# Optimization experiments

Hardware: AMD Instinct MI355X
Metric: run time of the kernel (lower is better)

The kernel has to match this reference:

```python
import jax, jax.numpy as jnp
import numpy as np

D, H, KVH, HD, FF = 768, 12, 4, 64, 2048
N_REP = H // KVH
EPS = 1e-6


def rmsnorm(x, w):
    # Faithful to source: norm = ||x|| * n^{-1/2}; eps added to norm (not inside sqrt)
    norm = jnp.sqrt(jnp.sum(x * x, axis=-1, keepdims=True)) * (x.shape[-1] ** -0.5)
    return w * x / (norm + EPS)


def rope_tables(seq_len, head_dim, base=10000.0):
    inv_freq = 1.0 / (base ** (np.arange(0, head_dim, 2, dtype=np.float32) / head_dim))
    t = np.arange(seq_len, dtype=np.float32)
    freqs = np.einsum('i,j->ij', t, inv_freq)  # [S, HD/2]
    emb = np.concatenate([freqs, freqs], axis=-1)  # [S, HD]
    return jnp.asarray(np.cos(emb)), jnp.asarray(np.sin(emb))


def rotate_half(x):
    h = x.shape[-1] // 2
    return jnp.concatenate([-x[..., h:], x[..., :h]], axis=-1)


def setup_inputs() -> dict:
    key = jax.random.key(0)
    ks = jax.random.split(key, 9)
    s = 0.02
    return {
        'x': jax.random.normal(ks[0], (2, 2048, D), jnp.float32),
        'Wq': jax.random.normal(ks[1], (H * HD, D), jnp.float32) * s,
        'Wk': jax.random.normal(ks[2], (KVH * HD, D), jnp.float32) * s,
        'Wv': jax.random.normal(ks[3], (KVH * HD, D), jnp.float32) * s,
        'Wo': jax.random.normal(ks[4], (D, H * HD), jnp.float32) * s,
        'Wgate': jax.random.normal(ks[5], (FF, D), jnp.float32) * s,
        'Wup': jax.random.normal(ks[6], (FF, D), jnp.float32) * s,
        'Wdown': jax.random.normal(ks[7], (D, FF), jnp.float32) * s,
        'g1': jnp.ones((D,), jnp.float32),
        'g2': jnp.ones((D,), jnp.float32),
    }


def reference(x, Wq, Wk, Wv, Wo, Wgate, Wup, Wdown, g1, g2):
    B, S, _ = x.shape
    # ---- attention sublayer (pre-norm) ----
    xn = rmsnorm(x, g1)
    q = (xn @ Wq.T).reshape(B, S, H, HD).transpose(0, 2, 1, 3)      # [B,H,S,HD]
    k = (xn @ Wk.T).reshape(B, S, KVH, HD).transpose(0, 2, 1, 3)    # [B,KVH,S,HD]
    v = (xn @ Wv.T).reshape(B, S, KVH, HD).transpose(0, 2, 1, 3)
    cos, sin = rope_tables(S, HD)                                   # [S,HD]
    q = q * cos + rotate_half(q) * sin
    k = k * cos + rotate_half(k) * sin
    # repeat kv heads to match q heads
    k = jnp.repeat(k, N_REP, axis=1)                                # [B,H,S,HD]
    v = jnp.repeat(v, N_REP, axis=1)
    scores = jnp.einsum('bhqd,bhkd->bhqk', q, k) / jnp.sqrt(jnp.float32(HD))
    causal = jnp.tril(jnp.ones((S, S), bool))
    scores = jnp.where(causal, scores, jnp.finfo(scores.dtype).min)
    attn = jax.nn.softmax(scores, axis=-1)
    out = jnp.einsum('bhqk,bhkd->bhqd', attn, v)                    # [B,H,S,HD]
    out = out.transpose(0, 2, 1, 3).reshape(B, S, H * HD) @ Wo.T
    x = x + out
    # ---- SwiGLU FFN sublayer (pre-norm) ----
    xn2 = rmsnorm(x, g2)
    ff = (jax.nn.silu(xn2 @ Wgate.T) * (xn2 @ Wup.T)) @ Wdown.T
    return x + ff
```

## Files before the change

### kernel.cpp

```cpp
#include <hip/hip_runtime.h>
#include <hip/hip_bf16.h>
#include <math.h>

typedef __bf16 bf16;
typedef __attribute__((ext_vector_type(8))) __bf16 bf16x8;
typedef __attribute__((ext_vector_type(4))) __bf16 bf16x4;
typedef __attribute__((ext_vector_type(4))) float f32x4;

#define MFMA16(a,b,c) __builtin_amdgcn_mfma_f32_16x16x32_bf16(a,b,c,0,0,0)

#define BATCH 2
#define SEQ   2048
#define DMODEL 768
#define NH    12
#define NKV   4
#define NREP  3
#define HD    64
#define FFDIM 2048
#define ROWS  (BATCH*SEQ)

#define QSCALE 0.18033688011112042f
#define LOG2E  1.4426950408889634f

#define WB(N) asm volatile("s_waitcnt vmcnt(" #N ")\n\ts_barrier" ::: "memory")
#define BAR() asm volatile("s_barrier" ::: "memory")

__device__ __forceinline__ void gl2lds16(const bf16* g, bf16* l) {
  __builtin_amdgcn_global_load_lds(
      (const __attribute__((address_space(1))) void*)g,
      (__attribute__((address_space(3))) void*)l, 16, 0, 0);
}

struct Cvt7 { const float* s[7]; bf16* d[7]; int n[7]; float* tab; };
__global__ __launch_bounds__(256) void cvt_all_kernel(Cvt7 c) {
  int seg = blockIdx.y;
  if (seg == 7) {
    int id = blockIdx.x * 256 + threadIdx.x;
    int j = id >> 11, s = id & 2047;
    float inv = expf(-(float)j * (9.210340371976184f / 32.0f));
    float ang = (float)s * inv;
    c.tab[id] = cosf(ang);
    c.tab[65536 + id] = sinf(ang);
    return;
  }
  const float* __restrict__ src = c.s[seg];
  bf16* __restrict__ dst = c.d[seg];
  int n = c.n[seg];
  int stride = gridDim.x * 256;
  if (seg == 4 || seg == 5) {
    int up = (seg == 5) ? 32 : 0;
    for (int i = blockIdx.x * 256 + threadIdx.x; i < n; i += stride) {
      int rg = i / 768, cc = i - rg * 768;
      int drow = ((rg >> 5) << 6) + (rg & 31) + up;
      dst[(size_t)drow * 768 + cc] = (bf16)src[i];
    }
    return;
  }
  for (int i = blockIdx.x * 256 + threadIdx.x; i < n; i += stride)
    dst[i] = (bf16)src[i];
}

__global__ __launch_bounds__(192) void rmsnorm_kernel(const float* __restrict__ x,
    const float* __restrict__ g, bf16* __restrict__ out) {
  int row = blockIdx.x;
  const float* xr = x + (size_t)row * DMODEL;
  int t = threadIdx.x;
  f32x4 v = *(const f32x4*)(xr + t * 4);
  float ss = v[0] * v[0] + v[1] * v[1] + v[2] * v[2] + v[3] * v[3];
  #pragma unroll
  for (int off = 32; off; off >>= 1) ss += __shfl_xor(ss, off, 64);
  __shared__ float red[3];
  if ((t & 63) == 0) red[t >> 6] = ss;
  __syncthreads();
  float total = red[0] + red[1] + red[2];
  float norm = sqrtf(total) * 0.03608439182435161f;
  float sc = 1.0f / (norm + 1e-6f);
  f32x4 gv = *(const f32x4*)(g + t * 4);
  bf16x4 o;
  #pragma unroll
  for (int i = 0; i < 4; ++i) o[i] = (bf16)(gv[i] * v[i] * sc);
  *(bf16x4*)(out + (size_t)row * DMODEL + t * 4) = o;
}

__global__ __launch_bounds__(512, 6) void gemm_out_kernel(const bf16* __restrict__ A,
    const bf16* __restrict__ B, float* __restrict__ C, const float* __restrict__ R,
    int N, int K) {
  __shared__ __align__(16) bf16 At[2][3][64 * 32];
  __shared__ __align__(16) bf16 Bt[2][3][64 * 32];
  int t = threadIdx.x;
  int g = t >> 8;
  int tt = t & 255;
  int lane = t & 63;
  int w = (t >> 6) & 3;
  int l15 = lane & 15, lq = lane >> 4;
  int wrow = (w >> 1) * 32, wcol = (w & 1) * 32;

  int flat = blockIdx.y * 12 + blockIdx.x;
  int f2 = (flat & 7) * 96 + (flat >> 3);
  int col0 = (f2 % 12) * 64, row0 = (f2 / 12) * 64;

  const int KH = K >> 1;
  const int NS = KH / 32;
  const bf16* Ag = A + (size_t)(row0 + (tt >> 2)) * K + g * KH + (tt & 3) * 8;
  const bf16* Bg = B + (size_t)(col0 + (tt >> 2)) * K + g * KH + (tt & 3) * 8;

  #pragma unroll
  for (int s = 0; s < 2; ++s) {
    gl2lds16(Ag + s * 32, At[g][s] + tt * 8);
    gl2lds16(Bg + s * 32, Bt[g][s] + tt * 8);
  }

  f32x4 zero = {0.f, 0.f, 0.f, 0.f};
  f32x4 acc[2][2];
  #pragma unroll
  for (int m = 0; m < 2; ++m)
    #pragma unroll
    for (int n = 0; n < 2; ++n) acc[m][n] = zero;

  #define OG_COMPUTE(slot) do {                                              \
    const bf16* at = At[g][slot]; const bf16* bt = Bt[g][slot];              \
    bf16x8 af[2], bb[2];                                                     \
    _Pragma("unroll")                                                        \
    for (int m = 0; m < 2; ++m)                                              \
      af[m] = *(const bf16x8*)(at + (wrow + m * 16 + l15) * 32 + lq * 8);    \
    _Pragma("unroll")                                                        \
    for (int n = 0; n < 2; ++n)                                              \
      bb[n] = *(const bf16x8*)(bt + (wcol + n * 16 + l15) * 32 + lq * 8);    \
    _Pragma("unroll")                                                        \
    for (int m = 0; m < 2; ++m)                                              \
      _Pragma("unroll")                                                      \
      for (int n = 0; n < 2; ++n)                                            \
        acc[m][n] = MFMA16(af[m], bb[n], acc[m][n]);                         \
  } while (0)

  int slot = 0;
  for (int k = 0; k < NS - 1; ++k) {
    WB(2);
    if (k + 2 < NS) {
      int ks = (k + 2) * 32;
      int ws = slot + 2; if (ws >= 3) ws -= 3;
      gl2lds16(Ag + ks, At[g][ws] + tt * 8);
      gl2lds16(Bg + ks, Bt[g][ws] + tt * 8);
    }
    OG_COMPUTE(slot);
    slot = (slot == 2) ? 0 : slot + 1;
  }
  WB(0);
  OG_COMPUTE(slot);
  #undef OG_COMPUTE

  __syncthreads();
  float* Cl = (float*)&At[0][0][0];
  if (g == 1) {
    #pragma unroll
    for (int m = 0; m < 2; ++m)
      #pragma unroll
      for (int n = 0; n < 2; ++n)
        #pragma unroll
        for (int r = 0; r < 4; ++r)
          Cl[(wrow + m * 16 + lq * 4 + r) * 64 + wcol + n * 16 + l15] = acc[m][n][r];
  }
  __syncthreads();
  if (g == 0) {
    #pragma unroll
    for (int m = 0; m < 2; ++m)
      #pragma unroll
      for (int n = 0; n < 2; ++n)
        #pragma unroll
        for (int r = 0; r < 4; ++r) {
          int row = wrow + m * 16 + lq * 4 + r;
          int col = wcol + n * 16 + l15;
          size_t idx = (size_t)(row0 + row) * N + col0 + col;
          C[idx] = acc[m][n][r] + Cl[row * 64 + col] + R[idx];
        }
  }
}

__global__ __launch_bounds__(256) void gemm_qkv_kernel(const bf16* __restrict__ A,
    const bf16* __restrict__ Wcat, const float* __restrict__ tab,
    bf16* __restrict__ Qh, bf16* __restrict__ Kh, bf16* __restrict__ Vt) {
  __shared__ __align__(16) bf16 At[4][64 * 32];
  __shared__ __align__(16) bf16 Bt[4][128 * 32];
  const int K = DMODEL;
  int t = threadIdx.x, lane = t & 63, wave = t >> 6;
  int l15 = lane & 15, lq = lane >> 4;
  int wrow = (wave >> 1) * 32, wcol = (wave & 1) * 64;
  int row0 = blockIdx.y * 64, col0 = blockIdx.x * 128;
  const bf16* Ag  = A + (size_t)(row0 + (t >> 2)) * K + (t & 3) * 8;
  const bf16* Bg0 = Wcat + (size_t)(col0 + (t >> 2)) * K + (t & 3) * 8;
  const bf16* Bg1 = Bg0 + (size_t)64 * K;
  const int NS = K / 32;

  #pragma unroll
  for (int s = 0; s < 3; ++s) {
    int ks = s * 32;
    gl2lds16(Ag + ks,  At[s] + t * 8);
    gl2lds16(Bg0 + ks, Bt[s] + t * 8);
    gl2lds16(Bg1 + ks, Bt[s] + 2048 + t * 8);
  }

  f32x4 zero = {0.f, 0.f, 0.f, 0.f};
  f32x4 acc[2][4];
  #pragma unroll
  for (int m = 0; m < 2; ++m)
    #pragma unroll
    for (int n = 0; n < 4; ++n) acc[m][n] = zero;

  #define QK_COMPUTE(slot) do {                                              \
    const bf16* at = At[slot]; const bf16* bt = Bt[slot];                    \
    bf16x8 af[2], bfr[4];                                                    \
    _Pragma("unroll")                                                        \
    for (int m = 0; m < 2; ++m)                                              \
      af[m] = *(const bf16x8*)(at + (wrow + m * 16 + l15) * 32 + lq * 8);    \
    _Pragma("unroll")                                                        \
    for (int n = 0; n < 4; ++n)                                              \
      bfr[n] = *(const bf16x8*)(bt + (wcol + n * 16 + l15) * 32 + lq * 8);   \
    _Pragma("unroll")                                                        \
    for (int m = 0; m < 2; ++m)                                              \
      _Pragma("unroll")                                                      \
      for (int n = 0; n < 4; ++n)                                            \
        acc[m][n] = MFMA16(af[m], bfr[n], acc[m][n]);                        \
  } while (0)

  for (int k = 0; k < NS - 2; ++k) {
    WB(6);
    if (k + 3 < NS) {
      int ks = (k + 3) * 32;
      int ws = (k + 3) & 3;
      gl2lds16(Ag + ks,  At[ws] + t * 8);
      gl2lds16(Bg0 + ks, Bt[ws] + t * 8);
      gl2lds16(Bg1 + ks, Bt[ws] + 2048 + t * 8);
    }
    QK_COMPUTE(k & 3);
  }
  WB(3);
  QK_COMPUTE((NS - 2) & 3);
  WB(0);
  QK_COMPUTE((NS - 1) & 3);
  #undef QK_COMPUTE

  int b = row0 >> 11;
  int s0 = (row0 & 2047) + wrow + lq * 4;
  int colw = col0 + wcol;
  if (colw < 768) {
    int h = colw >> 6;
    f32x4 cv[2][2], sv[2][2];
    #pragma unroll
    for (int m = 0; m < 2; ++m)
      #pragma unroll
      for (int jh = 0; jh < 2; ++jh) {
        const float* cp = tab + (jh * 16 + l15) * 2048 + s0 + m * 16;
        cv[m][jh] = *(const f32x4*)cp;
        sv[m][jh] = *(const f32x4*)(cp + 65536);
      }
    #pragma unroll
    for (int m = 0; m < 2; ++m)
      #pragma unroll
      for (int n = 0; n < 4; ++n) {
        float sgn = (n < 2) ? -1.f : 1.f;
        #pragma unroll
        for (int r = 0; r < 4; ++r) {
          float c = cv[m][n & 1][r], si = sv[m][n & 1][r];
          float rp = (acc[m][n][r] * c + sgn * acc[m][n ^ 2][r] * si) * QSCALE;
          Qh[((size_t)(b * NH + h) * SEQ + s0 + m * 16 + r) * 64 + n * 16 + l15] = (bf16)rp;
        }
      }
  } else if (colw < 1024) {
    int kh = (colw - 768) >> 6;
    f32x4 cv[2][2], sv[2][2];
    #pragma unroll
    for (int m = 0; m < 2; ++m)
      #pragma unroll
      for (int jh = 0; jh < 2; ++jh) {
        const float* cp = tab + (jh * 16 + l15) * 2048 + s0 + m * 16;
        cv[m][jh] = *(const f32x4*)cp;
        sv[m][jh] = *(const f32x4*)(cp + 65536);
      }
    #pragma unroll
    for (int m = 0; m < 2; ++m)
      #pragma unroll
      for (int n = 0; n < 4; ++n) {
        float sgn = (n < 2) ? -1.f : 1.f;
        #pragma unroll
        for (int r = 0; r < 4; ++r) {
          float c = cv[m][n & 1][r], si = sv[m][n & 1][r];
          float rp = acc[m][n][r] * c + sgn * acc[m][n ^ 2][r] * si;
          Kh[((size_t)(b * NKV + kh) * SEQ + s0 + m * 16 + r) * 64 + n * 16 + l15] = (bf16)rp;
        }
      }
  } else {
    int vh = (colw - 1024) >> 6;
    #pragma unroll
    for (int m = 0; m < 2; ++m)
      #pragma unroll
      for (int n = 0; n < 4; ++n) {
        bf16x4 pv;
        #pragma unroll
        for (int r = 0; r < 4; ++r) pv[r] = (bf16)acc[m][n][r];
        *(bf16x4*)(Vt + ((size_t)(b * NKV + vh) * 64 + n * 16 + l15) * SEQ + s0 + m * 16) = pv;
      }
  }
}

__global__ __launch_bounds__(512, 2) void gemm_gu_kernel(const bf16* __restrict__ A,
    const bf16* __restrict__ W, bf16* __restrict__ H) {
  __shared__ __align__(16) bf16 Als[2 * 2 * 128 * 64];
  __shared__ __align__(16) bf16 Bls[2 * 2 * 128 * 64];
  const int NT = 12;
  int t = threadIdx.x, lane = t & 63, wave = t >> 6;
  int l15 = lane & 15, lq = lane >> 4;
  int lfrag = l15 * 32 + lq * 8;
  int wm = wave >> 2, wn = wave & 3;

  int flat = blockIdx.y * 16 + blockIdx.x;
  int f2 = (flat & 7) * 32 + (flat >> 3);
  int colb = f2 & 15, rowb = f2 >> 4;
  int row0 = rowb * 256, col0w = colb * 256;

  #define STAGE(G, orow, L, j, h) do {                                       \
    bf16* lb = (L) + ((j) & 1) * 16384 + (h) * 8192 + t * 8;                 \
    const bf16* gb = (G) + (size_t)((orow) + (h) * 128 + ((t >> 7) << 4)     \
                   + ((t >> 2) & 15)) * 768 + (j) * 64                       \
                   + ((t >> 6) & 1) * 32 + (t & 3) * 8;                      \
    gl2lds16(gb, lb);                                                        \
    gl2lds16(gb + (size_t)64 * 768, lb + 4096);                              \
  } while (0)

  STAGE(W, col0w, Bls, 0, 0);  STAGE(W, col0w, Bls, 0, 1);
  STAGE(A, row0,  Als, 0, 0);  STAGE(A, row0,  Als, 0, 1);
  STAGE(W, col0w, Bls, 1, 0);  STAGE(W, col0w, Bls, 1, 1);

  f32x4 zero = {0.f, 0.f, 0.f, 0.f};
  f32x4 acc[8][4];
  #pragma unroll
  for (int m = 0; m < 8; ++m)
    #pragma unroll
    for (int n = 0; n < 4; ++n) acc[m][n] = zero;

  WB(4);

  for (int j = 0; j < NT; ++j) {
    const bf16* aB = Als + (j & 1) * 16384 + wm * 8192 + lfrag;
    const bf16* bB = Bls + (j & 1) * 16384 + (wn >> 1) * 8192 + (wn & 1) * 4096 + lfrag;
    bf16x8 afr[4][2], bfr[4][2];

    #pragma unroll
    for (int m = 0; m < 4; ++m)
      #pragma unroll
      for (int kk = 0; kk < 2; ++kk)
        afr[m][kk] = *(const bf16x8*)(aB + m * 1024 + kk * 512);
    #pragma unroll
    for (int n = 0; n < 2; ++n)
      #pragma unroll
      for (int kk = 0; kk < 2; ++kk)
        bfr[n][kk] = *(const bf16x8*)(bB + n * 1024 + kk * 512);
    if (j + 1 < NT) STAGE(A, row0, Als, j + 1, 0);
    BAR();
    __builtin_amdgcn_s_setprio(1);
    #pragma unroll
    for (int m = 0; m < 4; ++m)
      #pragma unroll
      for (int n = 0; n < 2; ++n) {
        acc[m][n] = MFMA16(afr[m][0], bfr[n][0], acc[m][n]);
        acc[m][n] = MFMA16(afr[m][1], bfr[n][1], acc[m][n]);
      }
    __builtin_amdgcn_s_setprio(0);
    BAR();

    #pragma unroll
    for (int n = 2; n < 4; ++n)
      #pragma unroll
      for (int kk = 0; kk < 2; ++kk)
        bfr[n][kk] = *(const bf16x8*)(bB + n * 1024 + kk * 512);
    if (j + 1 < NT) STAGE(A, row0, Als, j + 1, 1);
    BAR();
    __builtin_amdgcn_s_setprio(1);
    #pragma unroll
    for (int m = 0; m < 4; ++m)
      #pragma unroll
      for (int n = 2; n < 4; ++n) {
        acc[m][n] = MFMA16(afr[m][0], bfr[n][0], acc[m][n]);
        acc[m][n] = MFMA16(afr[m][1], bfr[n][1], acc[m][n]);
      }
    __builtin_amdgcn_s_setprio(0);
    BAR();

    #pragma unroll
    for (int m = 0; m < 4; ++m)
      #pragma unroll
      for (int kk = 0; kk < 2; ++kk)
        afr[m][kk] = *(const bf16x8*)(aB + (m + 4) * 1024 + kk * 512);
    if (j + 2 < NT) STAGE(W, col0w, Bls, j + 2, 0);
    BAR();
    __builtin_amdgcn_s_setprio(1);
    #pragma unroll
    for (int m = 0; m < 4; ++m)
      #pragma unroll
      for (int n = 0; n < 2; ++n) {
        acc[m + 4][n] = MFMA16(afr[m][0], bfr[n][0], acc[m + 4][n]);
        acc[m + 4][n] = MFMA16(afr[m][1], bfr[n][1], acc[m + 4][n]);
      }
    __builtin_amdgcn_s_setprio(0);
    BAR();

    if (j + 2 < NT) STAGE(W, col0w, Bls, j + 2, 1);
    BAR();
    __builtin_amdgcn_s_setprio(1);
    #pragma unroll
    for (int m = 0; m < 4; ++m)
      #pragma unroll
      for (int n = 2; n < 4; ++n) {
        acc[m + 4][n] = MFMA16(afr[m][0], bfr[n][0], acc[m + 4][n]);
        acc[m + 4][n] = MFMA16(afr[m][1], bfr[n][1], acc[m + 4][n]);
      }
    __builtin_amdgcn_s_setprio(0);
    if (j < NT - 2)       WB(4);
    else if (j == NT - 2) WB(0);
  }
  #undef STAGE

  int hc0 = colb * 128 + wn * 32;
  #pragma unroll
  for (int m = 0; m < 8; ++m)
    #pragma unroll
    for (int n = 0; n < 2; ++n)
      #pragma unroll
      for (int r = 0; r < 4; ++r) {
        int row = row0 + wm * 128 + m * 16 + lq * 4 + r;
        int col = hc0 + n * 16 + l15;
        float g = acc[m][n][r], u = acc[m][n + 2][r];
        float sg = g / (1.f + __builtin_amdgcn_exp2f(-g * LOG2E));
        H[(size_t)row * FFDIM + col] = (bf16)(sg * u);
      }
}

__global__ __launch_bounds__(256) void attn_kernel(const bf16* __restrict__ Qh,
    const bf16* __restrict__ Kh, const bf16* __restrict__ Vt, bf16* __restrict__ out) {
  __shared__ __align__(16) bf16 Kl0[2][64 * 32];
  __shared__ __align__(16) bf16 Kl1[2][64 * 32];
  __shared__ __align__(16) bf16 Vl0[2][64 * 32];
  __shared__ __align__(16) bf16 Vl1[2][64 * 32];
  __shared__ __align__(16) bf16 P[4][16 * 80];

  int idx = blockIdx.x;
  int qt = 31 - (idx / 24);
  int bh = idx % 24;
  int q0blk = qt * 64;
  int b = bh / NH, h = bh % NH;
  int kvh = h / NREP;
  int t = threadIdx.x;
  int lane = t & 63, wave = t >> 6;
  int l15 = lane & 15, lq = lane >> 4;
  int qw = q0blk + wave * 16;
  const bf16* Qb = Qh + (size_t)(b * NH + h) * SEQ * 64;
  const bf16* Kb = Kh + (size_t)(b * NKV + kvh) * SEQ * 64;
  const bf16* Vb = Vt + (size_t)(b * NKV + kvh) * 64 * SEQ;

  bf16x8 bq0 = *(const bf16x8*)(Qb + (size_t)(qw + l15) * 64 + lq * 8);
  bf16x8 bq1 = *(const bf16x8*)(Qb + (size_t)(qw + l15) * 64 + 32 + lq * 8);

  int srow = (t >> 6) * 16 + ((t >> 2) & 15);
  int scol = (t & 3) * 8;
  const bf16* Kg = Kb + (size_t)srow * 64 + scol;
  const bf16* Vg = Vb + (size_t)srow * SEQ + scol;
  bf16* Pw = P[wave];
  int Pwq = l15 * 80, lq8 = lq * 8, lq4 = lq * 4;
  int lfrag = l15 * 32 + lq8;
  const int NS = qt + 1;

  #pragma unroll
  for (int s = 0; s < 2; ++s) {
    int ks = (s < NS ? s : NS - 1) * 64;
    gl2lds16(Kg + (size_t)ks * 64,      Kl0[s] + t * 8);
    gl2lds16(Kg + (size_t)ks * 64 + 32, Kl1[s] + t * 8);
    gl2lds16(Vg + ks,                   Vl0[s] + t * 8);
    gl2lds16(Vg + ks + 32,              Vl1[s] + t * 8);
  }

  f32x4 zero = {0.f, 0.f, 0.f, 0.f};
  f32x4 o[4];
  o[0] = zero; o[1] = zero; o[2] = zero; o[3] = zero;
  float l_r = 0.f;

  #define ATTN_STEP(kk, slot) do {                                           \
    int k0 = (kk) * 64;                                                      \
    const bf16* kl0 = Kl0[slot]; const bf16* kl1 = Kl1[slot];                \
    const bf16* vl0 = Vl0[slot]; const bf16* vl1 = Vl1[slot];                \
    f32x4 s[4];                                                              \
    _Pragma("unroll")                                                        \
    for (int c = 0; c < 4; ++c) {                                            \
      bf16x8 ak0 = *(const bf16x8*)(kl0 + c * 512 + lfrag);                  \
      bf16x8 ak1 = *(const bf16x8*)(kl1 + c * 512 + lfrag);                  \
      s[c] = zero;                                                           \
      s[c] = MFMA16(ak0, bq0, s[c]);                                         \
      s[c] = MFMA16(ak1, bq1, s[c]);                                         \
    }                                                                        \
    if (k0 + 63 > qw) {                                                      \
      int qmk = qw + l15 - k0 - lq4;                                         \
      _Pragma("unroll")                                                      \
      for (int c = 0; c < 4; ++c)                                            \
        _Pragma("unroll")                                                    \
        for (int r = 0; r < 4; ++r)                                          \
          if (c * 16 + r > qmk) s[c][r] = -INFINITY;                         \
    }                                                                        \
    _Pragma("unroll")                                                        \
    for (int c = 0; c < 4; ++c) {                                            \
      bf16x4 pe;                                                             \
      _Pragma("unroll")                                                      \
      for (int r = 0; r < 4; ++r) {                                          \
        float e = __builtin_amdgcn_exp2f(s[c][r]);                           \
        l_r += e;                                                            \
        pe[r] = (bf16)e;                                                     \
      }                                                                      \
      *(bf16x4*)(Pw + Pwq + c * 16 + lq4) = pe;                              \
    }                                                                        \
    bf16x8 bp0 = *(const bf16x8*)(Pw + Pwq + lq8);                           \
    bf16x8 bp1 = *(const bf16x8*)(Pw + Pwq + 32 + lq8);                      \
    _Pragma("unroll")                                                        \
    for (int n = 0; n < 4; ++n) {                                            \
      bf16x8 av0 = *(const bf16x8*)(vl0 + n * 512 + lfrag);                  \
      bf16x8 av1 = *(const bf16x8*)(vl1 + n * 512 + lfrag);                  \
      o[n] = MFMA16(av0, bp0, o[n]);                                         \
      o[n] = MFMA16(av1, bp1, o[n]);                                         \
    }                                                                        \
  } while (0)

  for (int k = 0; k < NS - 1; ++k) {
    WB(4);
    ATTN_STEP(k, k & 1);
    BAR();
    if (k <= NS - 3) {
      int ks = (k + 2) * 64;
      gl2lds16(Kg + (size_t)ks * 64,      Kl0[k & 1] + t * 8);
      gl2lds16(Kg + (size_t)ks * 64 + 32, Kl1[k & 1] + t * 8);
      gl2lds16(Vg + ks,                   Vl0[k & 1] + t * 8);
      gl2lds16(Vg + ks + 32,              Vl1[k & 1] + t * 8);
    }
  }
  {
    WB(0);
    ATTN_STEP(NS - 1, (NS - 1) & 1);
  }
  #undef ATTN_STEP

  float lt = l_r;
  lt += __shfl_xor(lt, 16, 64);
  lt += __shfl_xor(lt, 32, 64);
  float inv = 1.f / lt;
  int q = qw + l15;
  bf16* orow = out + (size_t)(b * SEQ + q) * DMODEL + h * 64;
  #pragma unroll
  for (int n = 0; n < 4; ++n) {
    bf16x4 po;
    #pragma unroll
    for (int r = 0; r < 4; ++r) po[r] = (bf16)(o[n][r] * inv);
    *(bf16x4*)(orow + n * 16 + lq4) = po;
  }
}

extern "C" void kernel_launch(void* const* d_in, const int* in_sizes, int n_in,
                              void* d_out, int out_size, void* d_ws, size_t ws_size,
                              hipStream_t stream) {
  const float* x     = (const float*)d_in[0];
  const float* Wq    = (const float*)d_in[1];
  const float* Wk    = (const float*)d_in[2];
  const float* Wv    = (const float*)d_in[3];
  const float* Wo    = (const float*)d_in[4];
  const float* Wgate = (const float*)d_in[5];
  const float* Wup   = (const float*)d_in[6];
  const float* Wdown = (const float*)d_in[7];
  const float* g1    = (const float*)d_in[8];
  const float* g2    = (const float*)d_in[9];
  float* out = (float*)d_out;

  char* ws = (char*)d_ws;
  size_t off = 0;
  auto alloc = [&](size_t bytes) { size_t o = off; off += (bytes + 255) & ~(size_t)255; return o; };
  size_t o_tab  = alloc((size_t)2 * 32 * 2048 * 4);
  size_t o_x1   = alloc((size_t)4096 * 768 * 4);
  size_t o_xn   = alloc((size_t)4096 * 768 * 2);
  size_t o_Qh   = alloc((size_t)2 * 12 * 2048 * 64 * 2);
  size_t o_Kh   = alloc((size_t)2 * 4 * 2048 * 64 * 2);
  size_t o_Vt   = alloc((size_t)2 * 4 * 64 * 2048 * 2);
  size_t o_ao   = alloc((size_t)4096 * 768 * 2);
  size_t o_H    = alloc((size_t)4096 * 2048 * 2);
  size_t o_Wcat = alloc((size_t)1280 * 768 * 2);
  size_t o_Wo   = alloc((size_t)768 * 768 * 2);
  size_t o_Wgu  = alloc((size_t)4096 * 768 * 2);
  size_t o_Wdn  = alloc((size_t)768 * 2048 * 2);
  if (ws_size < off) return;

  float* tab  = (float*)(ws + o_tab);
  float* fx1  = (float*)(ws + o_x1);
  bf16* bxn   = (bf16*)(ws + o_xn);
  bf16* bQh   = (bf16*)(ws + o_Qh);
  bf16* bKh   = (bf16*)(ws + o_Kh);
  bf16* bVt   = (bf16*)(ws + o_Vt);
  bf16* bao   = (bf16*)(ws + o_ao);
  bf16* bH    = (bf16*)(ws + o_H);
  bf16* bWcat = (bf16*)(ws + o_Wcat);
  bf16* bWo   = (bf16*)(ws + o_Wo);
  bf16* bWgu  = (bf16*)(ws + o_Wgu);
  bf16* bWdn  = (bf16*)(ws + o_Wdn);

  Cvt7 c;
  c.s[0] = Wq;    c.d[0] = bWcat;              c.n[0] = 768 * 768;
  c.s[1] = Wk;    c.d[1] = bWcat + 768 * 768;  c.n[1] = 256 * 768;
  c.s[2] = Wv;    c.d[2] = bWcat + 1024 * 768; c.n[2] = 256 * 768;
  c.s[3] = Wo;    c.d[3] = bWo;                c.n[3] = 768 * 768;
  c.s[4] = Wgate; c.d[4] = bWgu;               c.n[4] = 2048 * 768;
  c.s[5] = Wup;   c.d[5] = bWgu;               c.n[5] = 2048 * 768;
  c.s[6] = Wdown; c.d[6] = bWdn;               c.n[6] = 768 * 2048;
  c.tab = tab;
  cvt_all_kernel<<<dim3(256, 8), 256, 0, stream>>>(c);

  rmsnorm_kernel<<<4096, 192, 0, stream>>>(x, g1, bxn);
  gemm_qkv_kernel<<<dim3(10, 64), 256, 0, stream>>>(bxn, bWcat, tab, bQh, bKh, bVt);
  attn_kernel<<<dim3(768), 256, 0, stream>>>(bQh, bKh, bVt, bao);
  gemm_out_kernel<<<dim3(12, 64), 512, 0, stream>>>(bao, bWo, fx1, x, 768, 768);

  rmsnorm_kernel<<<4096, 192, 0, stream>>>(fx1, g2, bxn);
  gemm_gu_kernel<<<dim3(16, 16), 512, 0, stream>>>(bxn, bWgu, bH);
  gemm_out_kernel<<<dim3(12, 64), 512, 0, stream>>>(bH, bWdn, out, fx1, 768, 2048);
}
```

Measured before the change: 240.5 us.

## Double attention query tile to 128 rows with 8 waves sharing K/V tiles

The attention kernel now processes 128 query rows per block using 512 threads (8 waves), so each K/V tile loaded into shared memory is reused by twice as many query rows. The grid is halved to 384 blocks, and each thread issues one K and one V async load per stage instead of two each. This halves global K/V traffic per query but gives coarser causal load balance and fewer blocks. It also wastes some masked work, since all waves iterate to the block's last key tile.

```diff
diff --git a/kernel.cpp b/kernel.cpp
--- a/kernel.cpp
+++ b/kernel.cpp
@@ -434,18 +434,16 @@
       }
 }
 
-__global__ __launch_bounds__(256) void attn_kernel(const bf16* __restrict__ Qh,
+__global__ __launch_bounds__(512) void attn_kernel(const bf16* __restrict__ Qh,
     const bf16* __restrict__ Kh, const bf16* __restrict__ Vt, bf16* __restrict__ out) {
-  __shared__ __align__(16) bf16 Kl0[2][64 * 32];
-  __shared__ __align__(16) bf16 Kl1[2][64 * 32];
-  __shared__ __align__(16) bf16 Vl0[2][64 * 32];
-  __shared__ __align__(16) bf16 Vl1[2][64 * 32];
-  __shared__ __align__(16) bf16 P[4][16 * 80];
+  __shared__ __align__(16) bf16 Kl[2][64 * 64];
+  __shared__ __align__(16) bf16 Vl[2][64 * 64];
+  __shared__ __align__(16) bf16 P[8][16 * 80];
 
   int idx = blockIdx.x;
-  int qt = 31 - (idx / 24);
+  int qt = 15 - (idx / 24);
   int bh = idx % 24;
-  int q0blk = qt * 64;
+  int q0blk = qt * 128;
   int b = bh / NH, h = bh % NH;
   int kvh = h / NREP;
   int t = threadIdx.x;
@@ -459,22 +457,20 @@
   bf16x8 bq0 = *(const bf16x8*)(Qb + (size_t)(qw + l15) * 64 + lq * 8);
   bf16x8 bq1 = *(const bf16x8*)(Qb + (size_t)(qw + l15) * 64 + 32 + lq * 8);
 
-  int srow = (t >> 6) * 16 + ((t >> 2) & 15);
-  int scol = (t & 3) * 8;
+  int srow = ((t >> 7) << 4) + ((t >> 2) & 15);
+  int scol = ((t >> 6) & 1) * 32 + (t & 3) * 8;
   const bf16* Kg = Kb + (size_t)srow * 64 + scol;
   const bf16* Vg = Vb + (size_t)srow * SEQ + scol;
   bf16* Pw = P[wave];
   int Pwq = l15 * 80, lq8 = lq * 8, lq4 = lq * 4;
   int lfrag = l15 * 32 + lq8;
-  const int NS = qt + 1;
+  const int NS = 2 * (qt + 1);
 
   #pragma unroll
   for (int s = 0; s < 2; ++s) {
-    int ks = (s < NS ? s : NS - 1) * 64;
-    gl2lds16(Kg + (size_t)ks * 64,      Kl0[s] + t * 8);
-    gl2lds16(Kg + (size_t)ks * 64 + 32, Kl1[s] + t * 8);
-    gl2lds16(Vg + ks,                   Vl0[s] + t * 8);
-    gl2lds16(Vg + ks + 32,              Vl1[s] + t * 8);
+    int ks = s * 64;
+    gl2lds16(Kg + (size_t)ks * 64, Kl[s] + t * 8);
+    gl2lds16(Vg + ks,              Vl[s] + t * 8);
   }
 
   f32x4 zero = {0.f, 0.f, 0.f, 0.f};
@@ -484,13 +480,12 @@
 
   #define ATTN_STEP(kk, slot) do {                                           \
     int k0 = (kk) * 64;                                                      \
-    const bf16* kl0 = Kl0[slot]; const bf16* kl1 = Kl1[slot];                \
-    const bf16* vl0 = Vl0[slot]; const bf16* vl1 = Vl1[slot];                \
+    const bf16* kl = Kl[slot]; const bf16* vl = Vl[slot];                    \
     f32x4 s[4];                                                              \
     _Pragma("unroll")                                                        \
     for (int c = 0; c < 4; ++c) {                                            \
-      bf16x8 ak0 = *(const bf16x8*)(kl0 + c * 512 + lfrag);                  \
-      bf16x8 ak1 = *(const bf16x8*)(kl1 + c * 512 + lfrag);                  \
+      bf16x8 ak0 = *(const bf16x8*)(kl + (c * 2 + 0) * 512 + lfrag);         \
+      bf16x8 ak1 = *(const bf16x8*)(kl + (c * 2 + 1) * 512 + lfrag);         \
       s[c] = zero;                                                           \
       s[c] = MFMA16(ak0, bq0, s[c]);                                         \
       s[c] = MFMA16(ak1, bq1, s[c]);                                         \
@@ -518,23 +513,21 @@
     bf16x8 bp1 = *(const bf16x8*)(Pw + Pwq + 32 + lq8);                      \
     _Pragma("unroll")                                                        \
     for (int n = 0; n < 4; ++n) {                                            \
-      bf16x8 av0 = *(const bf16x8*)(vl0 + n * 512 + lfrag);                  \
-      bf16x8 av1 = *(const bf16x8*)(vl1 + n * 512 + lfrag);                  \
+      bf16x8 av0 = *(const bf16x8*)(vl + (n * 2 + 0) * 512 + lfrag);         \
+      bf16x8 av1 = *(const bf16x8*)(vl + (n * 2 + 1) * 512 + lfrag);         \
       o[n] = MFMA16(av0, bp0, o[n]);                                         \
       o[n] = MFMA16(av1, bp1, o[n]);                                         \
     }                                                                        \
   } while (0)
 
   for (int k = 0; k < NS - 1; ++k) {
-    WB(4);
+    WB(2);
     ATTN_STEP(k, k & 1);
     BAR();
     if (k <= NS - 3) {
       int ks = (k + 2) * 64;
-      gl2lds16(Kg + (size_t)ks * 64,      Kl0[k & 1] + t * 8);
-      gl2lds16(Kg + (size_t)ks * 64 + 32, Kl1[k & 1] + t * 8);
-      gl2lds16(Vg + ks,                   Vl0[k & 1] + t * 8);
-      gl2lds16(Vg + ks + 32,              Vl1[k & 1] + t * 8);
+      gl2lds16(Kg + (size_t)ks * 64, Kl[k & 1] + t * 8);
+      gl2lds16(Vg + ks,              Vl[k & 1] + t * 8);
     }
   }
   {
@@ -616,7 +609,7 @@
 
   rmsnorm_kernel<<<4096, 192, 0, stream>>>(x, g1, bxn);
   gemm_qkv_kernel<<<dim3(10, 64), 256, 0, stream>>>(bxn, bWcat, tab, bQh, bKh, bVt);
-  attn_kernel<<<dim3(768), 256, 0, stream>>>(bQh, bKh, bVt, bao);
+  attn_kernel<<<dim3(384), 512, 0, stream>>>(bQh, bKh, bVt, bao);
   gemm_out_kernel<<<dim3(12, 64), 512, 0, stream>>>(bao, bWo, fx1, x, 768, 768);
 
   rmsnorm_kernel<<<4096, 192, 0, stream>>>(fx1, g2, bxn);
```

New measurement: 245.5 us. 1.02x slower.
